# Kernel tuning notes

Hardware: AMD Instinct MI355X
Metric: run time of the kernel (lower is better)

The kernel has to match this reference:

```python
import jax, jax.numpy as jnp
import numpy as np

B, IN, H, L, S = 256, 256, 256, 2, 128


def setup_inputs() -> dict:
    key = jax.random.key(0)
    ks = jax.random.split(key, 13)
    inp = {
        "x": jax.random.normal(ks[0], (B, IN), jnp.float32),
        "hidden_stack": jax.random.normal(ks[1], (S + 1, B, H, L), jnp.float32) * 0.1,
        "cell_stack": jax.random.normal(ks[2], (S + 1, B, H, L), jnp.float32) * 0.1,
        "w_ih0": jax.random.normal(ks[3], (4 * H, IN), jnp.float32) / np.sqrt(IN).astype(np.float32),
        "w_hh0": jax.random.normal(ks[4], (4 * H, H), jnp.float32) / np.sqrt(H).astype(np.float32),
        "b_ih0": jax.random.normal(ks[5], (4 * H,), jnp.float32) * 0.01,
        "b_hh0": jax.random.normal(ks[6], (4 * H,), jnp.float32) * 0.01,
        "w_ih1": jax.random.normal(ks[7], (4 * H, H), jnp.float32) / np.sqrt(H).astype(np.float32),
        "w_hh1": jax.random.normal(ks[8], (4 * H, H), jnp.float32) / np.sqrt(H).astype(np.float32),
        "b_ih1": jax.random.normal(ks[9], (4 * H,), jnp.float32) * 0.01,
        "b_hh1": jax.random.normal(ks[10], (4 * H,), jnp.float32) * 0.01,
        "op": jax.random.randint(ks[11], (B,), 0, 3, jnp.int32) - 1,  # {-1,0,1}: pop/hold/push
        "pos": jax.random.randint(ks[12], (B,), 1, S, jnp.int32),      # in-bounds for pos+1 and pos+op
    }
    return inp


def _lstm_cell(x, h, c, w_ih, w_hh, b_ih, b_hh):
    # torch.nn.LSTMCell gate order: input, forget, cell(g), output
    g = x @ w_ih.T + h @ w_hh.T + b_ih + b_hh  # (B, 4H)
    i, f, gg, o = jnp.split(g, 4, axis=-1)
    c2 = jax.nn.sigmoid(f) * c + jax.nn.sigmoid(i) * jnp.tanh(gg)
    h2 = jax.nn.sigmoid(o) * jnp.tanh(c2)
    return h2, c2


def reference(x, hidden_stack, cell_stack, w_ih0, w_hh0, b_ih0, b_hh0,
              w_ih1, w_hh1, b_ih1, b_hh1, op, pos):
    bidx = jnp.arange(x.shape[0])
    # gather current top-of-stack state: (B, H, L)
    cur_h = hidden_stack[pos, bidx]
    cur_c = cell_stack[pos, bidx]
    # two-layer LSTM cell (layer 1 feeds on layer 0 hidden)
    h0, c0 = _lstm_cell(x, cur_h[..., 0], cur_c[..., 0], w_ih0, w_hh0, b_ih0, b_hh0)
    h1, c1 = _lstm_cell(h0, cur_h[..., 1], cur_c[..., 1], w_ih1, w_hh1, b_ih1, b_hh1)
    next_h = jnp.stack([h0, h1], axis=-1)  # (B, H, L)
    next_c = jnp.stack([c0, c1], axis=-1)
    # scatter new state at pos+1
    hidden_stack = hidden_stack.at[pos + 1, bidx].set(next_h)
    cell_stack = cell_stack.at[pos + 1, bidx].set(next_c)
    # move stack pointer, gather return state
    new_pos = pos + op
    ret_h = hidden_stack[new_pos, bidx]  # (B, H, L)
    ret_c = cell_stack[new_pos, bidx]
    # faithful to torch source: hidden_ret[:, :, -1] -> shape (1, B, L)
    h_out = ret_h[:, -1, :][None]
    c_out = ret_c[:, -1, :][None]
    return h_out, c_out, hidden_stack, cell_stack
```

## Files before the change

### kernel.cpp

```cpp
#include <hip/hip_runtime.h>


static __device__ __forceinline__ float sigf(float x) {
    return 1.0f / (1.0f + __expf(-x));
}
static __device__ __forceinline__ float tanh_fast(float x) {
    return 2.0f / (1.0f + __expf(-2.0f * x)) - 1.0f;
}

__global__ __launch_bounds__(256) void gather_k(
    const float* __restrict__ x,
    const float* __restrict__ hid,
    const float* __restrict__ cel,
    const int* __restrict__ pos,
    float* __restrict__ A0, float* __restrict__ A1,
    float* __restrict__ c0in, float* __restrict__ c1in)
{
    int e = blockIdx.x * 256 + threadIdx.x;
    int b = e >> 8, h = e & 255;
    int p = pos[b];
    int base2 = ((p * 256 + b) * 256 + h) * 2;
    float2 hv = *(const float2*)&hid[base2];
    float2 cv = *(const float2*)&cel[base2];
    A0[b * 512 + h]       = x[e];
    A0[b * 512 + 256 + h] = hv.x;
    A1[b * 512 + 256 + h] = hv.y;
    c0in[e] = cv.x;
    c1in[e] = cv.y;
}

#define BM 32
#define BN 64
#define BK 16

__global__ __launch_bounds__(256) void gemm_k(
    const float* __restrict__ A,
    const float* __restrict__ wih,
    const float* __restrict__ whh,
    const float* __restrict__ bih,
    const float* __restrict__ bhh,
    float* __restrict__ gates)
{
    __shared__ float As[BK][BM + 2];
    __shared__ float Ws[BK][BN + 4];
    int t = threadIdx.x;
    int bm0 = (blockIdx.x >> 4) * BM;
    int jt0 = (blockIdx.x & 15) * BN;
    int am = t >> 3;
    int ac = (t & 7) * 2;
    int wr = t >> 2;
    int wc = (t & 3) * 4;
    int tx = t & 15, ty = t >> 4;
    float acc[2][4] = {{0.f,0.f,0.f,0.f},{0.f,0.f,0.f,0.f}};
    for (int kt = 0; kt < 512; kt += BK) {
        float2 av = *(const float2*)&A[(bm0 + am) * 512 + kt + ac];
        int j = jt0 + wr;
        int kk = kt + wc;
        const float* wsrc = (kk < 256) ? &wih[j * 256 + kk]
                                       : &whh[j * 256 + kk - 256];
        float4 wv = *(const float4*)wsrc;
        __syncthreads();
        As[ac][am]     = av.x;
        As[ac + 1][am] = av.y;
        Ws[wc][wr]     = wv.x;
        Ws[wc + 1][wr] = wv.y;
        Ws[wc + 2][wr] = wv.z;
        Ws[wc + 3][wr] = wv.w;
        __syncthreads();
        #pragma unroll
        for (int k = 0; k < BK; ++k) {
            float2 a  = *(const float2*)&As[k][ty * 2];
            float4 bv = *(const float4*)&Ws[k][tx * 4];
            acc[0][0] = fmaf(a.x, bv.x, acc[0][0]);
            acc[0][1] = fmaf(a.x, bv.y, acc[0][1]);
            acc[0][2] = fmaf(a.x, bv.z, acc[0][2]);
            acc[0][3] = fmaf(a.x, bv.w, acc[0][3]);
            acc[1][0] = fmaf(a.y, bv.x, acc[1][0]);
            acc[1][1] = fmaf(a.y, bv.y, acc[1][1]);
            acc[1][2] = fmaf(a.y, bv.z, acc[1][2]);
            acc[1][3] = fmaf(a.y, bv.w, acc[1][3]);
        }
    }
    #pragma unroll
    for (int m = 0; m < 2; ++m) {
        int b = bm0 + ty * 2 + m;
        #pragma unroll
        for (int n = 0; n < 4; ++n) {
            int j = jt0 + tx * 4 + n;
            gates[b * 1024 + j] = acc[m][n] + bih[j] + bhh[j];
        }
    }
}

__global__ __launch_bounds__(256) void act_k(
    const float* __restrict__ gates,
    const float* __restrict__ cin,
    float* __restrict__ hdst, int hstride,
    float* __restrict__ cdst)
{
    int e = blockIdx.x * 256 + threadIdx.x;
    int b = e >> 8, h = e & 255;
    const float* g = gates + b * 1024 + h;
    float gi = g[0], gf = g[256], gg = g[512], go = g[768];
    float c  = sigf(gf) * cin[e] + sigf(gi) * tanh_fast(gg);
    float hn = sigf(go) * tanh_fast(c);
    hdst[b * hstride + h] = hn;
    cdst[e] = c;
}

#define NV4_PER_STACK 4227072
#define NCOPY_BLOCKS  33024
#define STACK_ELEMS   16908288

__global__ __launch_bounds__(256) void copy_k(
    const float* __restrict__ hid, const float* __restrict__ cel,
    const int* __restrict__ pos, const int* __restrict__ op,
    const float* __restrict__ A1,
    const float* __restrict__ h1f,
    const float* __restrict__ c0f, const float* __restrict__ c1f,
    float* __restrict__ out)
{
    if (blockIdx.x == NCOPY_BLOCKS) {
        int b = threadIdx.x;
        int o = op[b];
        float h0v, h1v, c0v, c1v;
        if (o == 1) {
            h0v = A1[b * 512 + 255];
            h1v = h1f[b * 256 + 255];
            c0v = c0f[b * 256 + 255];
            c1v = c1f[b * 256 + 255];
        } else {
            int np = pos[b] + o;
            int base2 = ((np * 256 + b) * 256 + 255) * 2;
            h0v = hid[base2]; h1v = hid[base2 + 1];
            c0v = cel[base2]; c1v = cel[base2 + 1];
        }
        out[b * 2]           = h0v;
        out[b * 2 + 1]       = h1v;
        out[512 + b * 2]     = c0v;
        out[512 + b * 2 + 1] = c1v;
        return;
    }
    int v = blockIdx.x * 256 + threadIdx.x;
    bool is_cell = v >= NV4_PER_STACK;
    int vv = is_cell ? v - NV4_PER_STACK : v;
    int s   = vv >> 15;
    int rem = vv & 32767;
    int b   = rem >> 7;
    int q   = rem & 127;
    float4 val;
    if (s == pos[b] + 1) {
        int h = q * 2;
        const float* l0 = (is_cell ? (c0f + b * 256) : (A1 + b * 512)) + h;
        const float* l1 = (is_cell ? c1f : h1f) + b * 256 + h;
        val.x = l0[0]; val.y = l1[0];
        val.z = l0[1]; val.w = l1[1];
    } else {
        const float4* src = (const float4*)(is_cell ? cel : hid);
        val = src[vv];
    }
    float4* dst = (float4*)(out + 1024 + (is_cell ? STACK_ELEMS : 0));
    dst[vv] = val;
}

extern "C" void kernel_launch(void* const* d_in, const int* in_sizes, int n_in,
                              void* d_out, int out_size, void* d_ws, size_t ws_size,
                              hipStream_t stream) {
    const float* x    = (const float*)d_in[0];
    const float* hid  = (const float*)d_in[1];
    const float* cel  = (const float*)d_in[2];
    const float* wih0 = (const float*)d_in[3];
    const float* whh0 = (const float*)d_in[4];
    const float* bih0 = (const float*)d_in[5];
    const float* bhh0 = (const float*)d_in[6];
    const float* wih1 = (const float*)d_in[7];
    const float* whh1 = (const float*)d_in[8];
    const float* bih1 = (const float*)d_in[9];
    const float* bhh1 = (const float*)d_in[10];
    const int* op  = (const int*)d_in[11];
    const int* pos = (const int*)d_in[12];
    float* out = (float*)d_out;

    float* W    = (float*)d_ws;
    float* A0   = W;
    float* A1   = W + 131072;
    float* c0in = W + 262144;
    float* c1in = W + 327680;
    float* gates= W + 393216;
    float* c0f  = W + 655360;
    float* h1f  = W + 720896;
    float* c1f  = W + 786432;

    gather_k<<<256, 256, 0, stream>>>(x, hid, cel, pos, A0, A1, c0in, c1in);
    gemm_k<<<128, 256, 0, stream>>>(A0, wih0, whh0, bih0, bhh0, gates);
    act_k<<<256, 256, 0, stream>>>(gates, c0in, A1, 512, c0f);
    gemm_k<<<128, 256, 0, stream>>>(A1, wih1, whh1, bih1, bhh1, gates);
    act_k<<<256, 256, 0, stream>>>(gates, c1in, h1f, 256, c1f);
    copy_k<<<NCOPY_BLOCKS + 1, 256, 0, stream>>>(
        hid, cel, pos, op, A1, h1f, c0f, c1f, out);
}
```

Baseline: 312.2 us.

## Fuse gather into GEMM loads and layer-1 activation into stack copy

Removes the separate gather kernel by having the GEMM read x/h0 and the strided hidden stack directly via pos, and drops the second activation kernel by computing layer-1 LSTM outputs inside the copy kernel at the scatter slot. The GEMM tile changes to 16x64 with BK=32, register prefetch of the next tile, and vectorized bias/output stores, doubling the grid to 256 blocks. This cuts two launches and several workspace round trips, at the cost of strided uncoalesced reads of a_hi and duplicated activation math in the copy kernel.

```diff
diff --git a/kernel.cpp b/kernel.cpp
--- a/kernel.cpp
+++ b/kernel.cpp
@@ -8,130 +8,143 @@
     return 2.0f / (1.0f + __expf(-2.0f * x)) - 1.0f;
 }
 
-__global__ __launch_bounds__(256) void gather_k(
-    const float* __restrict__ x,
-    const float* __restrict__ hid,
-    const float* __restrict__ cel,
-    const int* __restrict__ pos,
-    float* __restrict__ A0, float* __restrict__ A1,
-    float* __restrict__ c0in, float* __restrict__ c1in)
-{
-    int e = blockIdx.x * 256 + threadIdx.x;
-    int b = e >> 8, h = e & 255;
-    int p = pos[b];
-    int base2 = ((p * 256 + b) * 256 + h) * 2;
-    float2 hv = *(const float2*)&hid[base2];
-    float2 cv = *(const float2*)&cel[base2];
-    A0[b * 512 + h]       = x[e];
-    A0[b * 512 + 256 + h] = hv.x;
-    A1[b * 512 + 256 + h] = hv.y;
-    c0in[e] = cv.x;
-    c1in[e] = cv.y;
-}
-
-#define BM 32
-#define BN 64
-#define BK 16
+#define GBM 16
+#define GBN 64
+#define GBK 32
 
 __global__ __launch_bounds__(256) void gemm_k(
-    const float* __restrict__ A,
+    const float* __restrict__ a_lo,
+    const float* __restrict__ a_hi,
+    const int*   __restrict__ pos,
     const float* __restrict__ wih,
     const float* __restrict__ whh,
     const float* __restrict__ bih,
     const float* __restrict__ bhh,
     float* __restrict__ gates)
 {
-    __shared__ float As[BK][BM + 2];
-    __shared__ float Ws[BK][BN + 4];
-    int t = threadIdx.x;
-    int bm0 = (blockIdx.x >> 4) * BM;
-    int jt0 = (blockIdx.x & 15) * BN;
-    int am = t >> 3;
-    int ac = (t & 7) * 2;
-    int wr = t >> 2;
-    int wc = (t & 3) * 4;
+    __shared__ float As[GBK][GBM + 1];
+    __shared__ float Ws[GBK][GBN + 4];
+    int t   = threadIdx.x;
+    int bm0 = (blockIdx.x >> 4) * GBM;
+    int jt0 = (blockIdx.x & 15) * GBN;
+    int arow = t >> 4;
+    int akk  = (t & 15) * 2;
+    int wrow = t >> 2;
+    int wkb  = (t & 3) * 8;
     int tx = t & 15, ty = t >> 4;
-    float acc[2][4] = {{0.f,0.f,0.f,0.f},{0.f,0.f,0.f,0.f}};
-    for (int kt = 0; kt < 512; kt += BK) {
-        float2 av = *(const float2*)&A[(bm0 + am) * 512 + kt + ac];
-        int j = jt0 + wr;
-        int kk = kt + wc;
-        const float* wsrc = (kk < 256) ? &wih[j * 256 + kk]
-                                       : &whh[j * 256 + kk - 256];
-        float4 wv = *(const float4*)wsrc;
+    int ab = bm0 + arow;
+    int ap = pos[ab];
+    int wj = jt0 + wrow;
+
+    float2 apre;
+    float4 wpre0, wpre1;
+    {
+        int k = akk;
+        apre = *(const float2*)&a_lo[ab * 256 + k];
+        const float* ws = &wih[wj * 256 + wkb];
+        wpre0 = *(const float4*)ws;
+        wpre1 = *(const float4*)(ws + 4);
+    }
+    float acc[4] = {0.f, 0.f, 0.f, 0.f};
+    for (int kt = 0; kt < 512; kt += GBK) {
         __syncthreads();
-        As[ac][am]     = av.x;
-        As[ac + 1][am] = av.y;
-        Ws[wc][wr]     = wv.x;
-        Ws[wc + 1][wr] = wv.y;
-        Ws[wc + 2][wr] = wv.z;
-        Ws[wc + 3][wr] = wv.w;
+        As[akk][arow]     = apre.x;
+        As[akk + 1][arow] = apre.y;
+        Ws[wkb][wrow]     = wpre0.x;
+        Ws[wkb + 1][wrow] = wpre0.y;
+        Ws[wkb + 2][wrow] = wpre0.z;
+        Ws[wkb + 3][wrow] = wpre0.w;
+        Ws[wkb + 4][wrow] = wpre1.x;
+        Ws[wkb + 5][wrow] = wpre1.y;
+        Ws[wkb + 6][wrow] = wpre1.z;
+        Ws[wkb + 7][wrow] = wpre1.w;
+        int kt2 = kt + GBK;
+        if (kt2 < 512) {
+            int k = kt2 + akk;
+            if (k < 256) {
+                apre = *(const float2*)&a_lo[ab * 256 + k];
+            } else {
+                const float* ah = a_hi + ((ap * 256 + ab) * 256 + (k - 256)) * 2;
+                apre.x = ah[0];
+                apre.y = ah[2];
+            }
+            int kk = kt2 + wkb;
+            const float* ws = (kk < 256) ? &wih[wj * 256 + kk]
+                                         : &whh[wj * 256 + kk - 256];
+            wpre0 = *(const float4*)ws;
+            wpre1 = *(const float4*)(ws + 4);
+        }
         __syncthreads();
         #pragma unroll
-        for (int k = 0; k < BK; ++k) {
-            float2 a  = *(const float2*)&As[k][ty * 2];
+        for (int k = 0; k < GBK; ++k) {
+            float a   = As[k][ty];
             float4 bv = *(const float4*)&Ws[k][tx * 4];
-            acc[0][0] = fmaf(a.x, bv.x, acc[0][0]);
-            acc[0][1] = fmaf(a.x, bv.y, acc[0][1]);
-            acc[0][2] = fmaf(a.x, bv.z, acc[0][2]);
-            acc[0][3] = fmaf(a.x, bv.w, acc[0][3]);
-            acc[1][0] = fmaf(a.y, bv.x, acc[1][0]);
-            acc[1][1] = fmaf(a.y, bv.y, acc[1][1]);
-            acc[1][2] = fmaf(a.y, bv.z, acc[1][2]);
-            acc[1][3] = fmaf(a.y, bv.w, acc[1][3]);
-        }
-    }
-    #pragma unroll
-    for (int m = 0; m < 2; ++m) {
-        int b = bm0 + ty * 2 + m;
-        #pragma unroll
-        for (int n = 0; n < 4; ++n) {
-            int j = jt0 + tx * 4 + n;
-            gates[b * 1024 + j] = acc[m][n] + bih[j] + bhh[j];
-        }
-    }
-}
-
-__global__ __launch_bounds__(256) void act_k(
+            acc[0] = fmaf(a, bv.x, acc[0]);
+            acc[1] = fmaf(a, bv.y, acc[1]);
+            acc[2] = fmaf(a, bv.z, acc[2]);
+            acc[3] = fmaf(a, bv.w, acc[3]);
+        }
+    }
+    int j = jt0 + tx * 4;
+    float4 b0 = *(const float4*)&bih[j];
+    float4 b1 = *(const float4*)&bhh[j];
+    float4 r;
+    r.x = acc[0] + b0.x + b1.x;
+    r.y = acc[1] + b0.y + b1.y;
+    r.z = acc[2] + b0.z + b1.z;
+    r.w = acc[3] + b0.w + b1.w;
+    *(float4*)&gates[(bm0 + ty) * 1024 + j] = r;
+}
+
+__global__ __launch_bounds__(256) void act0_k(
     const float* __restrict__ gates,
-    const float* __restrict__ cin,
-    float* __restrict__ hdst, int hstride,
-    float* __restrict__ cdst)
+    const float* __restrict__ cel,
+    const int*   __restrict__ pos,
+    float* __restrict__ h0f, float* __restrict__ c0f)
 {
     int e = blockIdx.x * 256 + threadIdx.x;
     int b = e >> 8, h = e & 255;
+    float cin = cel[((pos[b] * 256 + b) * 256 + h) * 2];
     const float* g = gates + b * 1024 + h;
     float gi = g[0], gf = g[256], gg = g[512], go = g[768];
-    float c  = sigf(gf) * cin[e] + sigf(gi) * tanh_fast(gg);
-    float hn = sigf(go) * tanh_fast(c);
-    hdst[b * hstride + h] = hn;
-    cdst[e] = c;
+    float c  = sigf(gf) * cin + sigf(gi) * tanh_fast(gg);
+    h0f[e] = sigf(go) * tanh_fast(c);
+    c0f[e] = c;
 }
 
 #define NV4_PER_STACK 4227072
 #define NCOPY_BLOCKS  33024
 #define STACK_ELEMS   16908288
 
+static __device__ __forceinline__ void lstm1(
+    const float* __restrict__ gates, const float* __restrict__ cel,
+    int p, int b, int h, float& hv, float& cv)
+{
+    float cin = cel[((p * 256 + b) * 256 + h) * 2 + 1];
+    const float* g = gates + b * 1024 + h;
+    float gi = g[0], gf = g[256], gg = g[512], go = g[768];
+    cv = sigf(gf) * cin + sigf(gi) * tanh_fast(gg);
+    hv = sigf(go) * tanh_fast(cv);
+}
+
 __global__ __launch_bounds__(256) void copy_k(
     const float* __restrict__ hid, const float* __restrict__ cel,
     const int* __restrict__ pos, const int* __restrict__ op,
-    const float* __restrict__ A1,
-    const float* __restrict__ h1f,
-    const float* __restrict__ c0f, const float* __restrict__ c1f,
+    const float* __restrict__ h0f, const float* __restrict__ c0f,
+    const float* __restrict__ gates,
     float* __restrict__ out)
 {
     if (blockIdx.x == NCOPY_BLOCKS) {
         int b = threadIdx.x;
         int o = op[b];
+        int p = pos[b];
         float h0v, h1v, c0v, c1v;
         if (o == 1) {
-            h0v = A1[b * 512 + 255];
-            h1v = h1f[b * 256 + 255];
+            h0v = h0f[b * 256 + 255];
             c0v = c0f[b * 256 + 255];
-            c1v = c1f[b * 256 + 255];
+            lstm1(gates, cel, p, b, 255, h1v, c1v);
         } else {
-            int np = pos[b] + o;
-            int base2 = ((np * 256 + b) * 256 + 255) * 2;
+            int base2 = (((p + o) * 256 + b) * 256 + 255) * 2;
             h0v = hid[base2]; h1v = hid[base2 + 1];
             c0v = cel[base2]; c1v = cel[base2 + 1];
         }
@@ -148,13 +161,20 @@
     int rem = vv & 32767;
     int b   = rem >> 7;
     int q   = rem & 127;
+    int p   = pos[b];
     float4 val;
-    if (s == pos[b] + 1) {
+    if (s == p + 1) {
         int h = q * 2;
-        const float* l0 = (is_cell ? (c0f + b * 256) : (A1 + b * 512)) + h;
-        const float* l1 = (is_cell ? c1f : h1f) + b * 256 + h;
-        val.x = l0[0]; val.y = l1[0];
-        val.z = l0[1]; val.w = l1[1];
+        float h1a, c1a, h1b, c1b;
+        lstm1(gates, cel, p, b, h,     h1a, c1a);
+        lstm1(gates, cel, p, b, h + 1, h1b, c1b);
+        if (is_cell) {
+            val.x = c0f[b * 256 + h];     val.y = c1a;
+            val.z = c0f[b * 256 + h + 1]; val.w = c1b;
+        } else {
+            val.x = h0f[b * 256 + h];     val.y = h1a;
+            val.z = h0f[b * 256 + h + 1]; val.w = h1b;
+        }
     } else {
         const float4* src = (const float4*)(is_cell ? cel : hid);
         val = src[vv];
@@ -182,20 +202,13 @@
     float* out = (float*)d_out;
 
     float* W    = (float*)d_ws;
-    float* A0   = W;
-    float* A1   = W + 131072;
-    float* c0in = W + 262144;
-    float* c1in = W + 327680;
-    float* gates= W + 393216;
-    float* c0f  = W + 655360;
-    float* h1f  = W + 720896;
-    float* c1f  = W + 786432;
-
-    gather_k<<<256, 256, 0, stream>>>(x, hid, cel, pos, A0, A1, c0in, c1in);
-    gemm_k<<<128, 256, 0, stream>>>(A0, wih0, whh0, bih0, bhh0, gates);
-    act_k<<<256, 256, 0, stream>>>(gates, c0in, A1, 512, c0f);
-    gemm_k<<<128, 256, 0, stream>>>(A1, wih1, whh1, bih1, bhh1, gates);
-    act_k<<<256, 256, 0, stream>>>(gates, c1in, h1f, 256, c1f);
+    float* gates= W;
+    float* h0f  = W + 262144;
+    float* c0f  = W + 327680;
+
+    gemm_k<<<256, 256, 0, stream>>>(x,   hid,     pos, wih0, whh0, bih0, bhh0, gates);
+    act0_k<<<256, 256, 0, stream>>>(gates, cel, pos, h0f, c0f);
+    gemm_k<<<256, 256, 0, stream>>>(h0f, hid + 1, pos, wih1, whh1, bih1, bhh1, gates);
     copy_k<<<NCOPY_BLOCKS + 1, 256, 0, stream>>>(
-        hid, cel, pos, op, A1, h1f, c0f, c1f, out);
-}
+        hid, cel, pos, op, h0f, c0f, gates, out);
+}
```

After: 284.8 us. -8.8%, faster.
